# Optimization experiments

Hardware: AMD Instinct MI355X
Metric: run time of the kernel (lower is better)

## Reference

```python
import jax, jax.numpy as jnp
import numpy as np
from jax import lax

B, T = 32, 1500
E, D, A, C, K, O = 512, 512, 512, 10, 100, 512
SCALING = 2.0


def setup_inputs() -> dict:
    key = jax.random.key(0)
    ks = jax.random.split(key, 12)
    inp = {
        "enc_pad": jax.random.normal(ks[0], (B, T, E), dtype=jnp.float32),
        "enc_len": jnp.full((B,), T, dtype=jnp.int32),
        "dec_z": jax.random.normal(ks[1], (B, D), dtype=jnp.float32),
        "att_prev": jax.random.uniform(ks[2], (B, T), dtype=jnp.float32) / T,
        # parameters (Linear weights stored as [in, out] for x @ W)
        "W_enc": jax.random.normal(ks[3], (E, A), dtype=jnp.float32) * (1.0 / np.sqrt(E)),
        "b_enc": jnp.zeros((A,), dtype=jnp.float32),
        "W_dec": jax.random.normal(ks[4], (D, A), dtype=jnp.float32) * (1.0 / np.sqrt(D)),
        "W_att": jax.random.normal(ks[5], (C, A), dtype=jnp.float32) * (1.0 / np.sqrt(C)),
        "conv_w": jax.random.normal(ks[6], (C, 1, 2 * K + 1), dtype=jnp.float32) * 0.05,  # OIH
        "gvec_w": jax.random.normal(ks[7], (A,), dtype=jnp.float32) * (1.0 / np.sqrt(A)),
        "W_o": jax.random.normal(ks[8], (E, O), dtype=jnp.float32) * (1.0 / np.sqrt(E)),
        "b_o": jnp.zeros((O,), dtype=jnp.float32),
    }
    return inp


def reference(enc_pad, enc_len, dec_z, att_prev, W_enc, b_enc, W_dec, W_att,
              conv_w, gvec_w, W_o, b_o):
    # pre_compute_enc_h = mlp_enc(enc_h): [B, T, A]
    pre_enc = jnp.einsum("bte,ea->bta", enc_pad, W_enc) + b_enc
    # location conv over previous attention weights: [B,1,T] -> [B,C,T]
    att_conv = lax.conv_general_dilated(
        att_prev[:, None, :], conv_w,
        window_strides=(1,), padding=[(K, K)],
        dimension_numbers=("NCH", "OIH", "NCH"))
    # [B, T, C] -> mlp_att -> [B, T, A]
    att_conv = jnp.einsum("bct,ca->bta", att_conv, W_att)
    # dec projection tiled: [B, 1, A]
    dec_tiled = (dec_z @ W_dec)[:, None, :]
    att_state = jnp.tanh(pre_enc + dec_tiled + att_conv)  # [B, T, A]
    e = jnp.einsum("bta,a->bt", att_state, gvec_w)          # [B, T]
    w = jax.nn.softmax(SCALING * e, axis=1)                  # [B, T]
    c = jnp.einsum("bt,bte->be", w, enc_pad)                 # [B, E]
    c = c @ W_o + b_o                                        # [B, O]
    return (c, w)
```

## Files before the change

### kernel.cpp

```cpp
#include <hip/hip_runtime.h>
#include <hip/hip_bf16.h>

#define B_  32
#define T_  1500
#define E_  512
#define A_  512
#define C_  10
#define KH  100
#define KW  201
#define O_  512
#define M_  (B_*T_)
#define KP  544
#define SCALING_ 2.0f
#define BT_BYTES 17408

typedef __bf16 bf16;
typedef __attribute__((ext_vector_type(8))) __bf16 bf16x8;
typedef __attribute__((ext_vector_type(4))) float f32x4;

__device__ __forceinline__ void load_lds16(const void* g, void* l) {
    __builtin_amdgcn_global_load_lds(
        (const __attribute__((address_space(1))) unsigned int*)g,
        (__attribute__((address_space(3))) unsigned int*)l,
        16, 0, 0);
}

__global__ void prep_bias(const float* __restrict__ dec_z, const float* __restrict__ W_dec,
                          const float* __restrict__ b_enc, float* __restrict__ bias) {
    int idx = blockIdx.x * 256 + threadIdx.x;
    int b = idx >> 9, a = idx & 511;
    float acc = b_enc[a];
#pragma unroll 8
    for (int d = 0; d < 512; ++d)
        acc += dec_z[b * 512 + d] * W_dec[d * 512 + a];
    bias[idx] = acc;
}

__global__ void prep_wt(const float* __restrict__ W_enc, const float* __restrict__ W_att,
                        bf16* __restrict__ wt2) {
    int k = blockIdx.x;
    int s = k >> 3, j = k & 7;
    for (int a = threadIdx.x; a < 512; a += 256) {
        float v;
        if (k < 512)       v = W_enc[k * 512 + a];
        else if (k < 522)  v = W_att[(k - 512) * 512 + a];
        else               v = 0.0f;
        int nt = a >> 4, c = a & 15;
        wt2[((nt * 68 + s) * 16 + c) * 8 + j] = (bf16)v;
    }
}

__global__ void prep_conv(const float* __restrict__ att_prev, const float* __restrict__ conv_w,
                          bf16* __restrict__ convpad) {
    int tc = blockIdx.x;
    int b  = blockIdx.y;
    int tid = threadIdx.x;
    __shared__ float s_att[456];
    __shared__ float s_w[C_ * KW];
    int t0 = tc * 256;
    for (int i = tid; i < 456; i += 256) {
        int ti = t0 - KH + i;
        s_att[i] = (ti >= 0 && ti < T_) ? att_prev[b * T_ + ti] : 0.0f;
    }
    for (int i = tid; i < C_ * KW; i += 256) s_w[i] = conv_w[i];
    __syncthreads();
    int t = t0 + tid;
    if (t < T_) {
        float acc[C_];
#pragma unroll
        for (int c = 0; c < C_; ++c) acc[c] = 0.0f;
        for (int j = 0; j < KW; ++j) {
            float a = s_att[tid + j];
#pragma unroll
            for (int c = 0; c < C_; ++c) acc[c] += a * s_w[c * KW + j];
        }
        bf16* dst = convpad + (size_t)(b * T_ + t) * 32;
#pragma unroll
        for (int c = 0; c < C_; ++c) dst[c] = (bf16)acc[c];
#pragma unroll
        for (int c = C_; c < 32; ++c) dst[c] = (bf16)0.0f;
    }
}

__global__ __launch_bounds__(256, 2) void main_gemm(
        const float* __restrict__ enc, const bf16* __restrict__ convpad,
        const bf16* __restrict__ wt2, const float* __restrict__ bias,
        const float* __restrict__ gvec, float* __restrict__ e_out) {
    __shared__ __align__(16) char b_lds[2 * BT_BYTES];
    const int tid  = threadIdx.x;
    const int lane = tid & 63;
    const int wid  = tid >> 6;
    const int g    = lane >> 4;
    const int c15  = lane & 15;
    const int rowbase = blockIdx.x * 128 + wid * 32;

    bf16x8 afrag[2][16];
#pragma unroll
    for (int m = 0; m < 2; ++m) {
        const float* ap = enc + (size_t)(rowbase + m * 16 + c15) * 512 + g * 8;
#pragma unroll
        for (int kt = 0; kt < 16; ++kt) {
            float4 f0 = *(const float4*)(ap + kt * 32);
            float4 f1 = *(const float4*)(ap + kt * 32 + 4);
            bf16x8 v;
            v[0] = (bf16)f0.x; v[1] = (bf16)f0.y; v[2] = (bf16)f0.z; v[3] = (bf16)f0.w;
            v[4] = (bf16)f1.x; v[5] = (bf16)f1.y; v[6] = (bf16)f1.z; v[7] = (bf16)f1.w;
            afrag[m][kt] = v;
        }
    }
    bf16x8 acv[2];
#pragma unroll
    for (int m = 0; m < 2; ++m)
        acv[m] = *(const bf16x8*)(convpad + (size_t)(rowbase + m * 16 + c15) * 32 + g * 8);

    int brw[2][4];
#pragma unroll
    for (int m = 0; m < 2; ++m)
#pragma unroll
        for (int r = 0; r < 4; ++r)
            brw[m][r] = ((rowbase + m * 16 + g * 4 + r) / T_) * 512;

    {
        const char* src = (const char*)wt2;
#pragma unroll
        for (int p = 0; p < 4; ++p) {
            int q = wid + p * 4;
            load_lds16(src + q * 1024 + lane * 16, b_lds + q * 1024);
        }
        if (wid == 0) load_lds16(src + 16 * 1024 + lane * 16, b_lds + 16 * 1024);
    }

    const int lane_off = g * 256 + c15 * 16;
    float s[2][4] = {{0.f,0.f,0.f,0.f},{0.f,0.f,0.f,0.f}};

    for (int nt = 0; nt < 32; ++nt) {
        __syncthreads();
        if (nt < 31) {
            const char* src = (const char*)wt2 + (size_t)(nt + 1) * BT_BYTES;
            char* dst = b_lds + ((nt + 1) & 1) * BT_BYTES;
#pragma unroll
            for (int p = 0; p < 4; ++p) {
                int q = wid + p * 4;
                load_lds16(src + q * 1024 + lane * 16, dst + q * 1024);
            }
            if (wid == 0) load_lds16(src + 16 * 1024 + lane * 16, dst + 16 * 1024);
        }
        const char* bb = b_lds + (nt & 1) * BT_BYTES + lane_off;
        f32x4 acc0 = {0.f, 0.f, 0.f, 0.f};
        f32x4 acc1 = {0.f, 0.f, 0.f, 0.f};
#pragma unroll
        for (int kt = 0; kt < 16; ++kt) {
            bf16x8 bv = *(const bf16x8*)(bb + kt * 1024);
            acc0 = __builtin_amdgcn_mfma_f32_16x16x32_bf16(afrag[0][kt], bv, acc0, 0, 0, 0);
            acc1 = __builtin_amdgcn_mfma_f32_16x16x32_bf16(afrag[1][kt], bv, acc1, 0, 0, 0);
        }
        {
            bf16x8 bv = *(const bf16x8*)(bb + 16 * 1024);
            acc0 = __builtin_amdgcn_mfma_f32_16x16x32_bf16(acv[0], bv, acc0, 0, 0, 0);
            acc1 = __builtin_amdgcn_mfma_f32_16x16x32_bf16(acv[1], bv, acc1, 0, 0, 0);
        }
        int n = nt * 16 + c15;
        float gv = gvec[n];
#pragma unroll
        for (int m = 0; m < 2; ++m) {
            f32x4 a = m ? acc1 : acc0;
#pragma unroll
            for (int r = 0; r < 4; ++r) {
                float x  = a[r] + bias[brw[m][r] + n];
                float ex = __expf(2.0f * x);
                float th = 1.0f - __fdividef(2.0f, ex + 1.0f);
                s[m][r] += gv * th;
            }
        }
    }
#pragma unroll
    for (int msk = 1; msk < 16; msk <<= 1)
#pragma unroll
        for (int m = 0; m < 2; ++m)
#pragma unroll
            for (int r = 0; r < 4; ++r)
                s[m][r] += __shfl_xor(s[m][r], msk, 64);
    if (c15 == 0) {
#pragma unroll
        for (int m = 0; m < 2; ++m)
#pragma unroll
            for (int r = 0; r < 4; ++r)
                e_out[rowbase + m * 16 + g * 4 + r] = s[m][r];
    }
}

__global__ void softmax_k(const float* __restrict__ e_in, float* __restrict__ w_out) {
    int b = blockIdx.x, tid = threadIdx.x;
    __shared__ float red[256];
    float v[6];
    float mx = -1e30f;
#pragma unroll
    for (int i = 0; i < 6; ++i) {
        int t = i * 256 + tid;
        v[i] = (t < T_) ? SCALING_ * e_in[b * T_ + t] : -1e30f;
        mx = fmaxf(mx, v[i]);
    }
    red[tid] = mx; __syncthreads();
    for (int st = 128; st > 0; st >>= 1) {
        if (tid < st) red[tid] = fmaxf(red[tid], red[tid + st]);
        __syncthreads();
    }
    mx = red[0]; __syncthreads();
    float sum = 0.f;
#pragma unroll
    for (int i = 0; i < 6; ++i) { v[i] = __expf(v[i] - mx); sum += v[i]; }
    red[tid] = sum; __syncthreads();
    for (int st = 128; st > 0; st >>= 1) {
        if (tid < st) red[tid] += red[tid + st];
        __syncthreads();
    }
    float inv = 1.0f / red[0];
#pragma unroll
    for (int i = 0; i < 6; ++i) {
        int t = i * 256 + tid;
        if (t < T_) w_out[b * T_ + t] = v[i] * inv;
    }
}

__global__ void ctx_partial(const float* __restrict__ enc, const float* __restrict__ w,
                            float* __restrict__ partial) {
    int e  = blockIdx.x * 256 + threadIdx.x;
    int ty = blockIdx.y;
    int b  = blockIdx.z;
    int t0 = ty * 94;
    int t1 = min(t0 + 94, T_);
    float acc = 0.f;
#pragma unroll 8
    for (int t = t0; t < t1; ++t)
        acc += w[b * T_ + t] * enc[((size_t)b * T_ + t) * 512 + e];
    partial[(ty * 32 + b) * 512 + e] = acc;
}

__global__ void out_proj(const float* __restrict__ partial, const float* __restrict__ Wo,
                         const float* __restrict__ bo, float* __restrict__ out) {
    int b = blockIdx.x, tid = threadIdx.x;
    __shared__ float ctx[512];
    for (int e = tid; e < 512; e += 256) {
        float s = 0.f;
#pragma unroll
        for (int p = 0; p < 16; ++p) s += partial[(p * 32 + b) * 512 + e];
        ctx[e] = s;
    }
    __syncthreads();
    float a0 = bo[tid];
    float a1 = bo[tid + 256];
#pragma unroll 8
    for (int e = 0; e < 512; ++e) {
        float c = ctx[e];
        a0 += c * Wo[e * 512 + tid];
        a1 += c * Wo[e * 512 + tid + 256];
    }
    out[b * 512 + tid]       = a0;
    out[b * 512 + tid + 256] = a1;
}

extern "C" void kernel_launch(void* const* d_in, const int* in_sizes, int n_in,
                              void* d_out, int out_size, void* d_ws, size_t ws_size,
                              hipStream_t stream) {
    const float* enc      = (const float*)d_in[0];
    const float* dec_z    = (const float*)d_in[2];
    const float* att_prev = (const float*)d_in[3];
    const float* W_enc    = (const float*)d_in[4];
    const float* b_enc    = (const float*)d_in[5];
    const float* W_dec    = (const float*)d_in[6];
    const float* W_att    = (const float*)d_in[7];
    const float* conv_w   = (const float*)d_in[8];
    const float* gvec     = (const float*)d_in[9];
    const float* W_o      = (const float*)d_in[10];
    const float* b_o      = (const float*)d_in[11];

    char* ws = (char*)d_ws;
    float* bias    = (float*)(ws);
    float* e_buf   = (float*)(ws + 65536);
    float* partial = (float*)(ws);
    bf16*  convpad = (bf16*)(ws + 1048576);
    bf16*  wt2     = (bf16*)(ws + 4120576);

    float* c_out = (float*)d_out;
    float* w_out = c_out + B_ * O_;

    prep_bias<<<64, 256, 0, stream>>>(dec_z, W_dec, b_enc, bias);
    prep_wt<<<KP, 256, 0, stream>>>(W_enc, W_att, wt2);
    prep_conv<<<dim3(6, B_), 256, 0, stream>>>(att_prev, conv_w, convpad);
    main_gemm<<<M_ / 128, 256, 0, stream>>>(enc, convpad, wt2, bias, gvec, e_buf);
    softmax_k<<<B_, 256, 0, stream>>>(e_buf, w_out);
    ctx_partial<<<dim3(2, 16, B_), 256, 0, stream>>>(enc, w_out, partial);
    out_proj<<<B_, 256, 0, stream>>>(partial, W_o, b_o, c_out);
}
```

Baseline: 334.6 us.

## Split main GEMM across N halves and simplify tanh-dot via gvec-sum identity

The attention GEMM is split so each block handles only half of the 512 attention columns. That doubles the grid to 750 blocks for better CU coverage, and the two halves are combined with atomicAdd into a memset buffer. tanh is rewritten as 1-2/(1+exp(2x)), so the per-element epilogue becomes exp2 plus a reciprocal, with the scale folded into the bias and the constant term taken from a precomputed sum of gvec. Bias and gvec are staged in LDS, and out_proj is split over two blocks per batch. In exchange, each encoder row fragment is loaded and converted by two blocks, and extra launches (gsum, memset) and atomics are added.

Result: faster. 316.6 us (-5.4%).

```diff
diff --git a/kernel.cpp b/kernel.cpp
--- a/kernel.cpp
+++ b/kernel.cpp
@@ -3,16 +3,14 @@
 
 #define B_  32
 #define T_  1500
-#define E_  512
-#define A_  512
 #define C_  10
 #define KH  100
 #define KW  201
-#define O_  512
-#define M_  (B_*T_)
+#define M_  48000
 #define KP  544
 #define SCALING_ 2.0f
 #define BT_BYTES 17408
+#define C2L 2.8853900817779268f
 
 typedef __bf16 bf16;
 typedef __attribute__((ext_vector_type(8))) __bf16 bf16x8;
@@ -26,14 +24,26 @@
 }
 
 __global__ void prep_bias(const float* __restrict__ dec_z, const float* __restrict__ W_dec,
-                          const float* __restrict__ b_enc, float* __restrict__ bias) {
+                          const float* __restrict__ b_enc, float* __restrict__ biasC) {
     int idx = blockIdx.x * 256 + threadIdx.x;
     int b = idx >> 9, a = idx & 511;
     float acc = b_enc[a];
 #pragma unroll 8
     for (int d = 0; d < 512; ++d)
         acc += dec_z[b * 512 + d] * W_dec[d * 512 + a];
-    bias[idx] = acc;
+    biasC[idx] = acc * C2L;
+}
+
+__global__ void gsum_k(const float* __restrict__ g, float* __restrict__ gsum) {
+    __shared__ float red[256];
+    int h = blockIdx.x, tid = threadIdx.x;
+    red[tid] = g[h * 256 + tid];
+    __syncthreads();
+    for (int st = 128; st > 0; st >>= 1) {
+        if (tid < st) red[tid] += red[tid + st];
+        __syncthreads();
+    }
+    if (tid == 0) gsum[h] = red[0];
 }
 
 __global__ void prep_wt(const float* __restrict__ W_enc, const float* __restrict__ W_att,
@@ -84,15 +94,29 @@
 
 __global__ __launch_bounds__(256, 2) void main_gemm(
         const float* __restrict__ enc, const bf16* __restrict__ convpad,
-        const bf16* __restrict__ wt2, const float* __restrict__ bias,
-        const float* __restrict__ gvec, float* __restrict__ e_out) {
+        const bf16* __restrict__ wt2, const float* __restrict__ biasC,
+        const float* __restrict__ gvec, const float* __restrict__ gsum,
+        float* __restrict__ e_out) {
     __shared__ __align__(16) char b_lds[2 * BT_BYTES];
+    __shared__ float biasL[2][256];
+    __shared__ float gvL[256];
     const int tid  = threadIdx.x;
     const int lane = tid & 63;
     const int wid  = tid >> 6;
     const int g    = lane >> 4;
     const int c15  = lane & 15;
-    const int rowbase = blockIdx.x * 128 + wid * 32;
+    const int bid  = blockIdx.x;
+    const int nh   = bid & 1;
+    const int rc   = bid >> 1;
+    const int rowbase = rc * 128 + wid * 32;
+    const int nbase   = nh * 256;
+
+    {
+        int b0 = (rc * 128) / T_, b1 = (rc * 128 + 127) / T_;
+        biasL[0][tid] = biasC[b0 * 512 + nbase + tid];
+        biasL[1][tid] = biasC[b1 * 512 + nbase + tid];
+        gvL[tid]      = gvec[nbase + tid];
+    }
 
     bf16x8 afrag[2][16];
 #pragma unroll
@@ -113,15 +137,18 @@
     for (int m = 0; m < 2; ++m)
         acv[m] = *(const bf16x8*)(convpad + (size_t)(rowbase + m * 16 + c15) * 32 + g * 8);
 
-    int brw[2][4];
-#pragma unroll
-    for (int m = 0; m < 2; ++m)
-#pragma unroll
-        for (int r = 0; r < 4; ++r)
-            brw[m][r] = ((rowbase + m * 16 + g * 4 + r) / T_) * 512;
-
+    int bsel[2][4];
     {
-        const char* src = (const char*)wt2;
+        int b0lim = ((rc * 128) / T_ + 1) * T_;
+#pragma unroll
+        for (int m = 0; m < 2; ++m)
+#pragma unroll
+            for (int r = 0; r < 4; ++r)
+                bsel[m][r] = (rowbase + m * 16 + g * 4 + r >= b0lim) ? 256 : 0;
+    }
+
+    {
+        const char* src = (const char*)wt2 + (size_t)(nh * 16) * BT_BYTES;
 #pragma unroll
         for (int p = 0; p < 4; ++p) {
             int q = wid + p * 4;
@@ -131,12 +158,13 @@
     }
 
     const int lane_off = g * 256 + c15 * 16;
-    float s[2][4] = {{0.f,0.f,0.f,0.f},{0.f,0.f,0.f,0.f}};
-
-    for (int nt = 0; nt < 32; ++nt) {
+    const float* blf = &biasL[0][0];
+    float su[2][4] = {{0.f,0.f,0.f,0.f},{0.f,0.f,0.f,0.f}};
+
+    for (int nt = 0; nt < 16; ++nt) {
         __syncthreads();
-        if (nt < 31) {
-            const char* src = (const char*)wt2 + (size_t)(nt + 1) * BT_BYTES;
+        if (nt < 15) {
+            const char* src = (const char*)wt2 + (size_t)(nh * 16 + nt + 1) * BT_BYTES;
             char* dst = b_lds + ((nt + 1) & 1) * BT_BYTES;
 #pragma unroll
             for (int p = 0; p < 4; ++p) {
@@ -159,17 +187,17 @@
             acc0 = __builtin_amdgcn_mfma_f32_16x16x32_bf16(acv[0], bv, acc0, 0, 0, 0);
             acc1 = __builtin_amdgcn_mfma_f32_16x16x32_bf16(acv[1], bv, acc1, 0, 0, 0);
         }
-        int n = nt * 16 + c15;
-        float gv = gvec[n];
+        int nloc = nt * 16 + c15;
+        float gv = gvL[nloc];
 #pragma unroll
         for (int m = 0; m < 2; ++m) {
             f32x4 a = m ? acc1 : acc0;
 #pragma unroll
             for (int r = 0; r < 4; ++r) {
-                float x  = a[r] + bias[brw[m][r] + n];
-                float ex = __expf(2.0f * x);
-                float th = 1.0f - __fdividef(2.0f, ex + 1.0f);
-                s[m][r] += gv * th;
+                float t  = fmaf(a[r], C2L, blf[bsel[m][r] + nloc]);
+                float ex = exp2f(t);
+                float u  = __builtin_amdgcn_rcpf(ex + 1.0f);
+                su[m][r] = fmaf(gv, u, su[m][r]);
             }
         }
     }
@@ -179,13 +207,15 @@
         for (int m = 0; m < 2; ++m)
 #pragma unroll
             for (int r = 0; r < 4; ++r)
-                s[m][r] += __shfl_xor(s[m][r], msk, 64);
+                su[m][r] += __shfl_xor(su[m][r], msk, 64);
     if (c15 == 0) {
+        float gs = gsum[nh];
 #pragma unroll
         for (int m = 0; m < 2; ++m)
 #pragma unroll
             for (int r = 0; r < 4; ++r)
-                e_out[rowbase + m * 16 + g * 4 + r] = s[m][r];
+                atomicAdd(e_out + rowbase + m * 16 + g * 4 + r,
+                          gs - 2.0f * su[m][r]);
     }
 }
 
@@ -238,7 +268,7 @@
 
 __global__ void out_proj(const float* __restrict__ partial, const float* __restrict__ Wo,
                          const float* __restrict__ bo, float* __restrict__ out) {
-    int b = blockIdx.x, tid = threadIdx.x;
+    int b = blockIdx.x, half = blockIdx.y, tid = threadIdx.x;
     __shared__ float ctx[512];
     for (int e = tid; e < 512; e += 256) {
         float s = 0.f;
@@ -247,16 +277,12 @@
         ctx[e] = s;
     }
     __syncthreads();
-    float a0 = bo[tid];
-    float a1 = bo[tid + 256];
+    int o = half * 256 + tid;
+    float a0 = bo[o];
 #pragma unroll 8
-    for (int e = 0; e < 512; ++e) {
-        float c = ctx[e];
-        a0 += c * Wo[e * 512 + tid];
-        a1 += c * Wo[e * 512 + tid + 256];
-    }
-    out[b * 512 + tid]       = a0;
-    out[b * 512 + tid + 256] = a1;
+    for (int e = 0; e < 512; ++e)
+        a0 += ctx[e] * Wo[e * 512 + o];
+    out[b * 512 + o] = a0;
 }
 
 extern "C" void kernel_launch(void* const* d_in, const int* in_sizes, int n_in,
@@ -275,20 +301,23 @@
     const float* b_o      = (const float*)d_in[11];
 
     char* ws = (char*)d_ws;
-    float* bias    = (float*)(ws);
+    float* biasC   = (float*)(ws);
     float* e_buf   = (float*)(ws + 65536);
+    float* gsum    = (float*)(ws + 257536);
     float* partial = (float*)(ws);
     bf16*  convpad = (bf16*)(ws + 1048576);
     bf16*  wt2     = (bf16*)(ws + 4120576);
 
     float* c_out = (float*)d_out;
-    float* w_out = c_out + B_ * O_;
-
-    prep_bias<<<64, 256, 0, stream>>>(dec_z, W_dec, b_enc, bias);
+    float* w_out = c_out + B_ * 512;
+
+    prep_bias<<<64, 256, 0, stream>>>(dec_z, W_dec, b_enc, biasC);
+    gsum_k<<<2, 256, 0, stream>>>(gvec, gsum);
     prep_wt<<<KP, 256, 0, stream>>>(W_enc, W_att, wt2);
     prep_conv<<<dim3(6, B_), 256, 0, stream>>>(att_prev, conv_w, convpad);
-    main_gemm<<<M_ / 128, 256, 0, stream>>>(enc, convpad, wt2, bias, gvec, e_buf);
+    hipMemsetAsync(e_buf, 0, M_ * sizeof(float), stream);
+    main_gemm<<<750, 256, 0, stream>>>(enc, convpad, wt2, biasC, gvec, gsum, e_buf);
     softmax_k<<<B_, 256, 0, stream>>>(e_buf, w_out);
     ctx_partial<<<dim3(2, 16, B_), 256, 0, stream>>>(enc, w_out, partial);
-    out_proj<<<B_, 256, 0, stream>>>(partial, W_o, b_o, c_out);
-}
+    out_proj<<<dim3(B_, 2), 256, 0, stream>>>(partial, W_o, b_o, c_out);
+}
```
